# Optimization experiments

Hardware: AMD Instinct MI355X
Metric: run time of the kernel (lower is better)

## Reference

```python
import jax, jax.numpy as jnp
import numpy as np

N_NODES = 100000
N_EDGES = 2000000
H = 128


def setup_inputs() -> dict:
    key = jax.random.key(0)
    ks = jax.random.split(key, 5)
    z_src = jax.random.normal(ks[0], (N_NODES, H), dtype=jnp.float32)
    z_dst = jax.random.normal(ks[1], (N_NODES, H), dtype=jnp.float32)
    edge_label_index = jax.random.randint(ks[2], (2, N_EDGES), 0, N_NODES, dtype=jnp.int64)
    # Linear(2H, H) and Linear(H, 1) params (stored as [in, out] for x @ W)
    W1 = jax.random.normal(ks[3], (2 * H, H), dtype=jnp.float32) * (1.0 / np.sqrt(2 * H))
    b1 = jnp.zeros((H,), dtype=jnp.float32)
    W2 = jax.random.normal(ks[4], (H, 1), dtype=jnp.float32) * (1.0 / np.sqrt(H))
    b2 = jnp.zeros((1,), dtype=jnp.float32)
    return {"z_src": z_src, "z_dst": z_dst, "edge_label_index": edge_label_index,
            "W1": W1, "b1": b1, "W2": W2, "b2": b2}


def reference(z_src, z_dst, edge_label_index, W1, b1, W2, b2):
    row, col = edge_label_index[0], edge_label_index[1]
    # gather + concat -> [E, 2H]
    z = jnp.concatenate([z_src[row], z_dst[col]], axis=-1)
    h = jax.nn.relu(z @ W1 + b1)          # [E, H]
    out = h @ W2 + b2                     # [E, 1]
    return out.reshape(-1)
```

## Files before the change

kernel.cpp:

```cpp
#include <hip/hip_runtime.h>

#define HDIM 128
#define ZP   136
#define NBH  512

typedef __bf16 bf16_t;
typedef bf16_t bf16x8 __attribute__((ext_vector_type(8)));
typedef float  f32x4  __attribute__((ext_vector_type(4)));

__device__ __forceinline__ unsigned short f2bf_rne(float f) {
    unsigned int u = __float_as_uint(f);
    u += 0x7fffu + ((u >> 16) & 1u);
    return (unsigned short)(u >> 16);
}
__device__ __forceinline__ unsigned int pk_bf2(float a, float b) {
    return (unsigned int)f2bf_rne(a) | ((unsigned int)f2bf_rne(b) << 16);
}

__global__ __launch_bounds__(256) void convert_w1(
    const float* __restrict__ W1, unsigned short* __restrict__ Wt)
{
    const int o = blockIdx.x * 256 + threadIdx.x;
    const int g = o >> 14, rem = o & 16383, n = rem >> 7, k = rem & 127;
    Wt[o] = f2bf_rne(W1[g * 16384 + k * 128 + n]);
}

__global__ __launch_bounds__(256) void node_gemm_v3(
    const float* __restrict__ Zs, const float* __restrict__ Zd,
    const unsigned short* __restrict__ Wt, const float* __restrict__ b1,
    unsigned short* __restrict__ Abuf, unsigned short* __restrict__ Bbuf,
    int M)
{
    __shared__ unsigned short wlds[128 * ZP];

    const bool second = (blockIdx.x >= NBH);
    const float* __restrict__ Z          = second ? Zd : Zs;
    const unsigned short* __restrict__ W = Wt + (second ? 128 * 128 : 0);
    unsigned short* __restrict__ C       = second ? Bbuf : Abuf;
    const int bx = second ? (blockIdx.x - NBH) : blockIdx.x;
    const int t  = threadIdx.x;

    #pragma unroll
    for (int j = 0; j < 8; ++j) {
        const int u = t + 256 * j;
        const int n = u >> 4, c = u & 15;
        const uint4 v = *reinterpret_cast<const uint4*>(W + n * 128 + c * 8);
        *reinterpret_cast<uint4*>(wlds + n * ZP + c * 8) = v;
    }
    __syncthreads();

    const int lane = t & 63;
    const int wave = t >> 6;
    const int m    = lane & 15;
    const int quad = lane >> 4;

    const int ntiles = (M + 63) >> 6;
    for (int tile = bx; tile < ntiles; tile += NBH) {
        const int row0 = tile * 64;
        const int r    = row0 + wave * 16 + m;
        const int rc   = (r < M) ? r : (M - 1);
        const float* zrow = Z + (size_t)rc * HDIM;

        f32x4 acc[8] = {};
        #pragma unroll
        for (int ks = 0; ks < 4; ++ks) {
            const float4 v0 = *reinterpret_cast<const float4*>(zrow + ks * 32 + quad * 8);
            const float4 v1 = *reinterpret_cast<const float4*>(zrow + ks * 32 + quad * 8 + 4);
            union { unsigned int u[4]; bf16x8 h; } zf;
            zf.u[0] = pk_bf2(v0.x, v0.y);
            zf.u[1] = pk_bf2(v0.z, v0.w);
            zf.u[2] = pk_bf2(v1.x, v1.y);
            zf.u[3] = pk_bf2(v1.z, v1.w);
            #pragma unroll
            for (int ct = 0; ct < 8; ++ct) {
                const bf16x8 wf = *reinterpret_cast<const bf16x8*>(
                    wlds + (ct * 16 + m) * ZP + ks * 32 + quad * 8);
                acc[ct] = __builtin_amdgcn_mfma_f32_16x16x32_bf16(wf, zf.h, acc[ct], 0, 0, 0);
            }
        }

        if (r < M) {
            unsigned short* crow = C + (size_t)r * HDIM;
            #pragma unroll
            for (int ct = 0; ct < 8; ++ct) {
                const int col = ct * 16 + quad * 4;
                float4 bv = make_float4(0.f, 0.f, 0.f, 0.f);
                if (second) bv = *reinterpret_cast<const float4*>(b1 + col);
                uint2 o;
                o.x = pk_bf2(acc[ct][0] + bv.x, acc[ct][1] + bv.y);
                o.y = pk_bf2(acc[ct][2] + bv.z, acc[ct][3] + bv.w);
                *reinterpret_cast<uint2*>(crow + col) = o;
            }
        }
    }
}

__global__ __launch_bounds__(256) void edge_decode_bf16(
    const unsigned short* __restrict__ A, const unsigned short* __restrict__ Bm,
    const int* __restrict__ idx,
    const float* __restrict__ W2, const float* __restrict__ b2,
    float* __restrict__ out, int E)
{
    const int t   = threadIdx.x;
    const int sub = t & 15;
    const int grp = t >> 4;

    float w2r[8];
    #pragma unroll
    for (int i = 0; i < 8; ++i) w2r[i] = W2[sub * 8 + i];
    const float b2s = b2[0];

    const int stride = gridDim.x * 16;
    for (int e = blockIdx.x * 16 + grp; e < E; e += stride) {
        const int r = idx[e];
        const int c = idx[E + e];
        const uint4 av = *reinterpret_cast<const uint4*>(A  + (size_t)r * HDIM + sub * 8);
        const uint4 bv = *reinterpret_cast<const uint4*>(Bm + (size_t)c * HDIM + sub * 8);

        float s = 0.f;
        #pragma unroll
        for (int i = 0; i < 4; ++i) {
            const unsigned int ua = (&av.x)[i];
            const unsigned int ub = (&bv.x)[i];
            s += fmaxf(__uint_as_float(ua << 16)         + __uint_as_float(ub << 16),         0.f) * w2r[2 * i];
            s += fmaxf(__uint_as_float(ua & 0xffff0000u) + __uint_as_float(ub & 0xffff0000u), 0.f) * w2r[2 * i + 1];
        }
        s += __shfl_xor(s, 1);
        s += __shfl_xor(s, 2);
        s += __shfl_xor(s, 4);
        s += __shfl_xor(s, 8);
        if (sub == 0) out[e] = s + b2s;
    }
}

extern "C" void kernel_launch(void* const* d_in, const int* in_sizes, int n_in,
                              void* d_out, int out_size, void* d_ws, size_t ws_size,
                              hipStream_t stream)
{
    const float* z_src = (const float*)d_in[0];
    const float* z_dst = (const float*)d_in[1];
    const int*   eidx  = (const int*)d_in[2];
    const float* W1    = (const float*)d_in[3];
    const float* b1    = (const float*)d_in[4];
    const float* W2    = (const float*)d_in[5];
    const float* b2    = (const float*)d_in[6];
    float*       outp  = (float*)d_out;

    const int Nn = in_sizes[0] / HDIM;
    const int E  = in_sizes[2] / 2;

    unsigned short* Abuf = (unsigned short*)d_ws;
    unsigned short* Bbuf = Abuf + (size_t)Nn * HDIM;
    unsigned short* Wt   = Bbuf + (size_t)Nn * HDIM;

    convert_w1<<<128, 256, 0, stream>>>(W1, Wt);

    node_gemm_v3<<<2 * NBH, 256, 0, stream>>>(z_src, z_dst, Wt, b1, Abuf, Bbuf, Nn);

    edge_decode_bf16<<<8192, 256, 0, stream>>>(Abuf, Bbuf, eidx, W2, b2, outp, E);
}
```

Before: 292.8 us.

## Launch one node-GEMM block per tile, prefetch Z rows before weight staging, swizzle LDS

The node GEMM now launches one block per 64-row tile instead of a fixed 512-block grid-stride loop. Each block issues its global loads of the Z rows before staging the weights into LDS, so the load latency overlaps the weight copy. The padded LDS layout is replaced by an XOR-swizzled unpadded layout to avoid bank conflicts. In exchange, every block reloads the 32 KB weight tile into LDS (about 3100 blocks instead of 1024), which raises LDS-fill traffic.

```diff
diff --git a/kernel.cpp b/kernel.cpp
--- a/kernel.cpp
+++ b/kernel.cpp
@@ -1,8 +1,6 @@
 #include <hip/hip_runtime.h>
 
 #define HDIM 128
-#define ZP   136
-#define NBH  512
 
 typedef __bf16 bf16_t;
 typedef bf16_t bf16x8 __attribute__((ext_vector_type(8)));
@@ -25,72 +23,77 @@
     Wt[o] = f2bf_rne(W1[g * 16384 + k * 128 + n]);
 }
 
-__global__ __launch_bounds__(256) void node_gemm_v3(
+__global__ __launch_bounds__(256) void node_gemm_v6(
     const float* __restrict__ Zs, const float* __restrict__ Zd,
     const unsigned short* __restrict__ Wt, const float* __restrict__ b1,
     unsigned short* __restrict__ Abuf, unsigned short* __restrict__ Bbuf,
-    int M)
+    int M, int tiles_per_half)
 {
-    __shared__ unsigned short wlds[128 * ZP];
+    __shared__ unsigned short wlds[128 * 128];
 
-    const bool second = (blockIdx.x >= NBH);
+    const bool second = (blockIdx.x >= tiles_per_half);
+    const int tile = second ? (blockIdx.x - tiles_per_half) : blockIdx.x;
     const float* __restrict__ Z          = second ? Zd : Zs;
     const unsigned short* __restrict__ W = Wt + (second ? 128 * 128 : 0);
     unsigned short* __restrict__ C       = second ? Bbuf : Abuf;
-    const int bx = second ? (blockIdx.x - NBH) : blockIdx.x;
-    const int t  = threadIdx.x;
-
-    #pragma unroll
-    for (int j = 0; j < 8; ++j) {
-        const int u = t + 256 * j;
-        const int n = u >> 4, c = u & 15;
-        const uint4 v = *reinterpret_cast<const uint4*>(W + n * 128 + c * 8);
-        *reinterpret_cast<uint4*>(wlds + n * ZP + c * 8) = v;
-    }
-    __syncthreads();
-
+    const int t    = threadIdx.x;
     const int lane = t & 63;
     const int wave = t >> 6;
     const int m    = lane & 15;
     const int quad = lane >> 4;
 
-    const int ntiles = (M + 63) >> 6;
-    for (int tile = bx; tile < ntiles; tile += NBH) {
-        const int row0 = tile * 64;
-        const int r    = row0 + wave * 16 + m;
-        const int rc   = (r < M) ? r : (M - 1);
-        const float* zrow = Z + (size_t)rc * HDIM;
+    const int r  = tile * 64 + wave * 16 + m;
+    const int rc = (r < M) ? r : (M - 1);
+    const float* zrow = Z + (size_t)rc * HDIM;
+    float4 zv[4][2];
+    #pragma unroll
+    for (int ks = 0; ks < 4; ++ks) {
+        zv[ks][0] = *reinterpret_cast<const float4*>(zrow + ks * 32 + quad * 8);
+        zv[ks][1] = *reinterpret_cast<const float4*>(zrow + ks * 32 + quad * 8 + 4);
+    }
 
-        f32x4 acc[8] = {};
+    #pragma unroll
+    for (int j = 0; j < 8; ++j) {
+        const int u = t + 256 * j;
+        const int n = u >> 4, cc = u & 15;
+        const uint4 v = *reinterpret_cast<const uint4*>(W + n * 128 + cc * 8);
+        *reinterpret_cast<uint4*>(wlds + n * 128 + (cc ^ (n & 7)) * 8) = v;
+    }
+    __syncthreads();
+
+    union { unsigned int u[4]; bf16x8 h; } zf[4];
+    #pragma unroll
+    for (int ks = 0; ks < 4; ++ks) {
+        zf[ks].u[0] = pk_bf2(zv[ks][0].x, zv[ks][0].y);
+        zf[ks].u[1] = pk_bf2(zv[ks][0].z, zv[ks][0].w);
+        zf[ks].u[2] = pk_bf2(zv[ks][1].x, zv[ks][1].y);
+        zf[ks].u[3] = pk_bf2(zv[ks][1].z, zv[ks][1].w);
+    }
+
+    f32x4 acc[8] = {};
+    #pragma unroll
+    for (int ks = 0; ks < 4; ++ks) {
+        const int cidx = (ks * 4 + quad) ^ (m & 7);
         #pragma unroll
-        for (int ks = 0; ks < 4; ++ks) {
-            const float4 v0 = *reinterpret_cast<const float4*>(zrow + ks * 32 + quad * 8);
-            const float4 v1 = *reinterpret_cast<const float4*>(zrow + ks * 32 + quad * 8 + 4);
-            union { unsigned int u[4]; bf16x8 h; } zf;
-            zf.u[0] = pk_bf2(v0.x, v0.y);
-            zf.u[1] = pk_bf2(v0.z, v0.w);
-            zf.u[2] = pk_bf2(v1.x, v1.y);
-            zf.u[3] = pk_bf2(v1.z, v1.w);
-            #pragma unroll
-            for (int ct = 0; ct < 8; ++ct) {
-                const bf16x8 wf = *reinterpret_cast<const bf16x8*>(
-                    wlds + (ct * 16 + m) * ZP + ks * 32 + quad * 8);
-                acc[ct] = __builtin_amdgcn_mfma_f32_16x16x32_bf16(wf, zf.h, acc[ct], 0, 0, 0);
-            }
+        for (int ct = 0; ct < 8; ++ct) {
+            const bf16x8 wf = *reinterpret_cast<const bf16x8*>(
+                wlds + (ct * 16 + m) * 128 + cidx * 8);
+            acc[ct] = __builtin_amdgcn_mfma_f32_16x16x32_bf16(
+                wf, zf[ks].h, acc[ct], 0, 0, 0);
         }
+    }
 
-        if (r < M) {
-            unsigned short* crow = C + (size_t)r * HDIM;
-            #pragma unroll
-            for (int ct = 0; ct < 8; ++ct) {
-                const int col = ct * 16 + quad * 4;
-                float4 bv = make_float4(0.f, 0.f, 0.f, 0.f);
-                if (second) bv = *reinterpret_cast<const float4*>(b1 + col);
-                uint2 o;
-                o.x = pk_bf2(acc[ct][0] + bv.x, acc[ct][1] + bv.y);
-                o.y = pk_bf2(acc[ct][2] + bv.z, acc[ct][3] + bv.w);
-                *reinterpret_cast<uint2*>(crow + col) = o;
-            }
+    if (r < M) {
+        unsigned short* crow = C + (size_t)r * HDIM;
+        #pragma unroll
+        for (int ct = 0; ct < 8; ++ct) {
+            const int col = ct * 16 + quad * 4;
+            float4 bv = make_float4(0.f, 0.f, 0.f, 0.f);
+            if (second) bv = *reinterpret_cast<const float4*>(b1 + col);
+            uint2 o;
+            o.x = pk_bf2(acc[ct][0] + bv.x, acc[ct][1] + bv.y);
+            o.y = pk_bf2(acc[ct][2] + bv.z, acc[ct][3] + bv.w);
+            *reinterpret_cast<uint2*>(crow + col) = o;
         }
     }
 }
@@ -155,7 +158,9 @@
 
     convert_w1<<<128, 256, 0, stream>>>(W1, Wt);
 
-    node_gemm_v3<<<2 * NBH, 256, 0, stream>>>(z_src, z_dst, Wt, b1, Abuf, Bbuf, Nn);
+    const int tiles = (Nn + 63) >> 6;
+    node_gemm_v6<<<2 * tiles, 256, 0, stream>>>(
+        z_src, z_dst, Wt, b1, Abuf, Bbuf, Nn, tiles);
 
     edge_decode_bf16<<<8192, 256, 0, stream>>>(Abuf, Bbuf, eidx, W2, b2, outp, E);
 }
```

New measurement: 291.4 us. About the same (-0.5%).
